# Kernel tuning notes

Hardware: AMD Instinct MI355X
Metric: run time of the kernel (lower is better)

The kernel has to match this reference:

```python
import jax, jax.numpy as jnp
import numpy as np

EPS = 1e-8
N_ITER = 3
S = 8      # n_slots
D = 64     # slot_size
HID = 128  # mlp hidden


def _ln(x, w, b):
    m = jnp.mean(x, axis=-1, keepdims=True)
    v = jnp.var(x, axis=-1, keepdims=True)
    return (x - m) * jax.lax.rsqrt(v + 1e-5) * w + b


def setup_inputs() -> dict:
    key = jax.random.key(0)
    ks = jax.random.split(key, 20)
    B, N, Din = 128, 4096, 64
    g = lambda k, sh, s: (jax.random.normal(k, sh, jnp.float32) * s)
    return {
        "inputs": jax.random.normal(ks[0], (B, N, Din), jnp.float32),
        "eps_noise": jax.random.normal(ks[1], (B, S, D), jnp.float32),
        "slot_mu": g(ks[2], (1, 1, D), 0.1),
        "slot_logvar": g(ks[3], (1, 1, D), 0.1),
        "k_w": g(ks[4], (D, Din), 1.0 / np.sqrt(Din)),
        "v_w": g(ks[5], (D, Din), 1.0 / np.sqrt(Din)),
        "q_w": g(ks[6], (D, D), 1.0 / np.sqrt(D)),
        "ni_w": jnp.ones((Din,), jnp.float32), "ni_b": jnp.zeros((Din,), jnp.float32),
        "ns_w": jnp.ones((D,), jnp.float32),  "ns_b": jnp.zeros((D,), jnp.float32),
        "nr_w": jnp.ones((D,), jnp.float32),  "nr_b": jnp.zeros((D,), jnp.float32),
        "gru_wih": g(ks[7], (3 * D, D), 1.0 / np.sqrt(D)),
        "gru_whh": g(ks[8], (3 * D, D), 1.0 / np.sqrt(D)),
        "gru_bih": jnp.zeros((3 * D,), jnp.float32),
        "gru_bhh": jnp.zeros((3 * D,), jnp.float32),
        "mlp_w1": g(ks[9], (HID, D), 1.0 / np.sqrt(D)),
        "mlp_w2": g(ks[10], (D, HID), 1.0 / np.sqrt(HID)),
        "mlp_b2": jnp.zeros((D,), jnp.float32),
    }


def _gru(x, h, wih, whh, bih, bhh):
    gi = x @ wih.T + bih  # [BS, 3D]
    gh = h @ whh.T + bhh
    i_r, i_z, i_n = jnp.split(gi, 3, axis=-1)
    h_r, h_z, h_n = jnp.split(gh, 3, axis=-1)
    r = jax.nn.sigmoid(i_r + h_r)
    z = jax.nn.sigmoid(i_z + h_z)
    n = jnp.tanh(i_n + r * h_n)
    return (1.0 - z) * n + z * h


def _step(slots, k, v, q_w, ns_w, ns_b, nr_w, nr_b,
          gru_wih, gru_whh, gru_bih, gru_bhh, mlp_w1, mlp_w2, mlp_b2):
    B = slots.shape[0]
    q = _ln(slots, ns_w, ns_b) @ q_w.T                     # [B,S,D]
    logits = jnp.einsum('bnd,bsd->bns', k, q)              # [B,N,S]
    w = jax.nn.softmax(logits, axis=-1) + EPS              # softmax over slots
    w = w / jnp.sum(w, axis=-2, keepdims=True)             # renorm over tokens
    atten_maps = jnp.einsum('bns,bnd->bsd', w, v)          # [B,S,D]
    h = _gru(atten_maps.reshape(B * S, D), slots.reshape(B * S, D),
             gru_wih, gru_whh, gru_bih, gru_bhh)
    h = h + (jax.nn.relu(_ln(h, nr_w, nr_b) @ mlp_w1.T) @ mlp_w2.T + mlp_b2)
    return h.reshape(B, S, D), w


def reference(inputs, eps_noise, slot_mu, slot_logvar, k_w, v_w, q_w,
              ni_w, ni_b, ns_w, ns_b, nr_w, nr_b,
              gru_wih, gru_whh, gru_bih, gru_bhh, mlp_w1, mlp_w2, mlp_b2):
    std = jnp.exp(0.5 * slot_logvar)
    slots = slot_mu + std * eps_noise                      # [B,S,D]
    x = _ln(inputs, ni_w, ni_b)
    k = (x @ k_w.T) / np.sqrt(D).astype(np.float32)        # [B,N,D]
    v = x @ v_w.T
    args = (q_w, ns_w, ns_b, nr_w, nr_b, gru_wih, gru_whh,
            gru_bih, gru_bhh, mlp_w1, mlp_w2, mlp_b2)
    for _ in range(N_ITER):
        slots, w = _step(slots, k, v, *args)
    slots, w = _step(jax.lax.stop_gradient(slots), k, v, *args)
    return slots, w
```

## Files before the change

kernel.cpp:

```cpp
#include <hip/hip_runtime.h>
#include <hip/hip_bf16.h>

#define BB 128
#define NN 4096
#define DD 64
#define SS 8
#define HH 128

typedef __attribute__((ext_vector_type(8))) short short8;
typedef __attribute__((ext_vector_type(4))) short short4v;
typedef __attribute__((ext_vector_type(4))) float f32x4;

__device__ __forceinline__ float warp_red_sum(float v) {
    #pragma unroll
    for (int off = 32; off; off >>= 1) v += __shfl_xor(v, off);
    return v;
}

__device__ __forceinline__ float bcastlane(float v, int l) {
    return __int_as_float(__builtin_amdgcn_readlane(__float_as_int(v), l));
}

__device__ __forceinline__ unsigned short bfu(float f) {
    __hip_bfloat16 h = __float2bfloat16(f);
    return *(unsigned short*)&h;
}

__device__ __forceinline__ unsigned pk2(float a, float b) {
    return (unsigned)bfu(a) | ((unsigned)bfu(b) << 16);
}

__device__ __forceinline__ short4v ds_tr16(unsigned off) {
    short4v r;
    asm volatile("ds_read_b64_tr_b16 %0, %1" : "=v"(r) : "v"(off));
    return r;
}

__global__ __launch_bounds__(256) void prep_kernel(
    const float* __restrict__ v_w, const float* __restrict__ q_w,
    const float* __restrict__ wih, const float* __restrict__ whh,
    const float* __restrict__ w1, const float* __restrict__ w2,
    float* __restrict__ vwT, float* __restrict__ qwT,
    float* __restrict__ wihT, float* __restrict__ whhT,
    float* __restrict__ w1T, float* __restrict__ w2T)
{
    int i0 = blockIdx.x * blockDim.x + threadIdx.x;
    int nthr = gridDim.x * blockDim.x;
    for (int t = i0; t < 4096; t += nthr) {
        int i = t >> 6, o = t & 63;
        vwT[t] = v_w[o * 64 + i];
        qwT[t] = q_w[o * 64 + i];
    }
    for (int t = i0; t < 12288; t += nthr) {
        int r = t / 192, c = t % 192;
        wihT[t] = wih[c * 64 + r];
        whhT[t] = whh[c * 64 + r];
    }
    for (int t = i0; t < 8192; t += nthr) {
        int r = t >> 7, c = t & 127;
        w1T[t] = w1[c * 64 + r];
    }
    for (int t = i0; t < 8192; t += nthr) {
        int r = t >> 6, c = t & 63;
        w2T[t] = w2[c * 128 + r];
    }
}

__global__ __launch_bounds__(256) void init_q_kernel(
    const float* __restrict__ eps, const float* __restrict__ mu,
    const float* __restrict__ lv, const float* __restrict__ qwT,
    const float* __restrict__ k_w,
    const float* __restrict__ nsw, const float* __restrict__ nsb,
    float* __restrict__ slots, unsigned short* __restrict__ qb,
    float* __restrict__ zbuf)
{
    const int tid = threadIdx.x, lane = tid & 63;
    const int row = blockIdx.x * 4 + (tid >> 6);
    const int idx = row * 64 + lane;
    float s0 = mu[lane] + __expf(0.5f * lv[lane]) * eps[idx];
    slots[idx] = s0;
    float m = warp_red_sum(s0) * (1.0f / 64.0f);
    float dx = s0 - m;
    float var = warp_red_sum(dx * dx) * (1.0f / 64.0f);
    float xln = dx * rsqrtf(var + 1e-5f) * nsw[lane] + nsb[lane];
    float q = 0.f;
    #pragma unroll 8
    for (int i = 0; i < 64; ++i) q = fmaf(bcastlane(xln, i), qwT[i * 64 + lane], q);
    float qp = 0.f;
    #pragma unroll 8
    for (int o = 0; o < 64; ++o) qp = fmaf(bcastlane(q, o), k_w[o * 64 + lane], qp);
    qb[idx] = bfu(qp * 0.125f);
    int g = blockIdx.x * 256 + tid;
    for (int j = g; j < 66560; j += 65536) zbuf[j] = 0.f;
}

__global__ __launch_bounds__(256) void phase_a_ln(
    const float* __restrict__ inp, const float* __restrict__ niw, const float* __restrict__ nib,
    unsigned short* __restrict__ xb)
{
    const int tid = threadIdx.x, lane = tid & 63, widx = tid >> 6;
    const int t8 = lane >> 3, d8 = lane & 7;
    const float4 wn0 = *(const float4*)&niw[d8 * 8];
    const float4 wn1 = *(const float4*)&niw[d8 * 8 + 4];
    const float4 bn0 = *(const float4*)&nib[d8 * 8];
    const float4 bn1 = *(const float4*)&nib[d8 * 8 + 4];
    const int tok0 = blockIdx.x * 128;
    #pragma unroll
    for (int it = 0; it < 4; ++it) {
        const int m = widx * 32 + it * 8 + t8;
        const float* rowp = inp + (size_t)(tok0 + m) * 64 + d8 * 8;
        float4 a = *(const float4*)rowp;
        float4 c = *(const float4*)(rowp + 4);
        float s1 = (a.x + a.y + a.z + a.w) + (c.x + c.y + c.z + c.w);
        float s2 = fmaf(a.x, a.x, fmaf(a.y, a.y, fmaf(a.z, a.z, a.w * a.w)));
        s2 = fmaf(c.x, c.x, fmaf(c.y, c.y, fmaf(c.z, c.z, fmaf(c.w, c.w, s2))));
        #pragma unroll
        for (int o = 1; o < 8; o <<= 1) { s1 += __shfl_xor(s1, o); s2 += __shfl_xor(s2, o); }
        float mean = s1 * (1.0f / 64.0f);
        float var = s2 * (1.0f / 64.0f) - mean * mean;
        float rstd = rsqrtf(var + 1e-5f);
        float y[8];
        y[0] = (a.x - mean) * rstd * wn0.x + bn0.x;
        y[1] = (a.y - mean) * rstd * wn0.y + bn0.y;
        y[2] = (a.z - mean) * rstd * wn0.z + bn0.z;
        y[3] = (a.w - mean) * rstd * wn0.w + bn0.w;
        y[4] = (c.x - mean) * rstd * wn1.x + bn1.x;
        y[5] = (c.y - mean) * rstd * wn1.y + bn1.y;
        y[6] = (c.z - mean) * rstd * wn1.z + bn1.z;
        y[7] = (c.w - mean) * rstd * wn1.w + bn1.w;
        uint4 o4;
        o4.x = pk2(y[0], y[1]); o4.y = pk2(y[2], y[3]);
        o4.z = pk2(y[4], y[5]); o4.w = pk2(y[6], y[7]);
        *(uint4*)&xb[(size_t)(tok0 + m) * 64 + d8 * 8] = o4;
    }
}

__global__ __launch_bounds__(256) void attn_mfma(
    const __hip_bfloat16* __restrict__ xb,
    const unsigned short* __restrict__ qb,
    float* __restrict__ numer, float* __restrict__ denom, float* __restrict__ wout)
{
    __shared__ unsigned short smem[11904];
    unsigned short* Qs = smem;
    const int tid = threadIdx.x, lane = tid & 63, widx = tid >> 6;
    unsigned short* wls = smem + 1152 + widx * 640;
    unsigned short* Xw  = smem + 3712 + widx * 2048;
    const int b = blockIdx.y;
    const int quad = lane >> 4, l16 = lane & 15;
    const int twave0 = blockIdx.x * 512 + widx * 128;

    short8 bkA[2][2], bkB[2][2];
    #pragma unroll
    for (int t4h = 0; t4h < 2; ++t4h) {
        const size_t xrow = ((size_t)b * NN + twave0 + t4h * 16 + l16) * 64;
        bkA[t4h][0] = *(const short8*)&xb[xrow + quad * 8];
        bkA[t4h][1] = *(const short8*)&xb[xrow + 32 + quad * 8];
    }

    for (int t = tid; t < 1024; t += 256) {
        int s = t >> 6, dd = t & 63;
        Qs[s * 72 + dd] = (s < 8) ? qb[b * 512 + t] : (unsigned short)0;
    }
    for (int t = lane; t < 320; t += 64) wls[320 + t] = 0;
    __syncthreads();

    short8 aq0 = *(const short8*)&Qs[l16 * 72 + quad * 8];
    short8 aq1 = *(const short8*)&Qs[l16 * 72 + 32 + quad * 8];

    f32x4 accv[4];
    #pragma unroll
    for (int nt = 0; nt < 4; ++nt) accv[nt] = (f32x4){0.f, 0.f, 0.f, 0.f};
    float dacc[4] = {0.f, 0.f, 0.f, 0.f};

    unsigned short* xw0 = Xw + (quad >> 1) * 512 + l16 * 16 + (quad & 1) * 8;
    const unsigned xtr = (unsigned)(size_t)Xw
                       + (unsigned)((quad * 8 + (l16 >> 2)) * 32 + (l16 & 3) * 8);

    auto PROC = [&](short8 (&cur)[2][2], short8 (&nxt)[2][2], int hg, bool pf) {
        const int t0g = twave0 + hg * 32;
        if (pf) {
            #pragma unroll
            for (int t4h = 0; t4h < 2; ++t4h) {
                const size_t xrow = ((size_t)b * NN + t0g + 32 + t4h * 16 + l16) * 64;
                nxt[t4h][0] = *(const short8*)&xb[xrow + quad * 8];
                nxt[t4h][1] = *(const short8*)&xb[xrow + 32 + quad * 8];
            }
        }
        #pragma unroll
        for (int t4h = 0; t4h < 2; ++t4h) {
            const int tok = t0g + t4h * 16 + l16;
            short8 bk0 = cur[t4h][0];
            short8 bk1 = cur[t4h][1];
            *(short8*)(xw0 + t4h * 256) = bk0;
            *(short8*)(xw0 + t4h * 256 + 1024) = bk1;
            f32x4 lg = (f32x4){0.f, 0.f, 0.f, 0.f};
            lg = __builtin_amdgcn_mfma_f32_16x16x32_bf16(aq0, bk0, lg, 0, 0, 0);
            lg = __builtin_amdgcn_mfma_f32_16x16x32_bf16(aq1, bk1, lg, 0, 0, 0);
            float e[4];
            #pragma unroll
            for (int r = 0; r < 4; ++r) e[r] = __expf(lg[r]);
            float s4 = (e[0] + e[1]) + (e[2] + e[3]);
            float stot = s4 + __shfl_xor(s4, 16);
            float rs = __builtin_amdgcn_rcpf(stot);
            float wv[4];
            #pragma unroll
            for (int r = 0; r < 4; ++r) { wv[r] = fmaf(e[r], rs, 1e-8f); dacc[r] += wv[r]; }
            if (quad < 2) {
                #pragma unroll
                for (int r = 0; r < 4; ++r)
                    wls[(quad * 4 + r) * 40 + t4h * 16 + l16] = bfu(wv[r]);
                if (wout)
                    *(float4*)&wout[((size_t)b * NN + tok) * 8 + quad * 4] =
                        make_float4(wv[0], wv[1], wv[2], wv[3]);
            }
        }
        asm volatile("" ::: "memory");
        short8 aw = *(const short8*)&wls[l16 * 40 + quad * 8];
        short4v rlo[4], rhi[4];
        #pragma unroll
        for (int nt = 0; nt < 4; ++nt) {
            rlo[nt] = ds_tr16(xtr + nt * 1024);
            rhi[nt] = ds_tr16(xtr + nt * 1024 + 128);
        }
        asm volatile("s_waitcnt lgkmcnt(0)");
        __builtin_amdgcn_sched_barrier(0);
        #pragma unroll
        for (int nt = 0; nt < 4; ++nt) {
            short8 bv = __builtin_shufflevector(rlo[nt], rhi[nt], 0, 1, 2, 3, 4, 5, 6, 7);
            accv[nt] = __builtin_amdgcn_mfma_f32_16x16x32_bf16(aw, bv, accv[nt], 0, 0, 0);
        }
    };

    PROC(bkA, bkB, 0, true);
    PROC(bkB, bkA, 1, true);
    PROC(bkA, bkB, 2, true);
    PROC(bkB, bkA, 3, false);

    #pragma unroll
    for (int r = 0; r < 4; ++r) {
        dacc[r] += __shfl_xor(dacc[r], 1);
        dacc[r] += __shfl_xor(dacc[r], 2);
        dacc[r] += __shfl_xor(dacc[r], 4);
        dacc[r] += __shfl_xor(dacc[r], 8);
    }
    __syncthreads();
    float* red = (float*)smem;
    float* dred = red + 2048;
    if (quad < 2) {
        #pragma unroll
        for (int nt = 0; nt < 4; ++nt)
            #pragma unroll
            for (int r = 0; r < 4; ++r)
                red[widx * 512 + (quad * 4 + r) * 64 + nt * 16 + l16] = accv[nt][r];
        if (l16 == 0) {
            #pragma unroll
            for (int r = 0; r < 4; ++r) dred[widx * 8 + quad * 4 + r] = dacc[r];
        }
    }
    __syncthreads();
    for (int e = tid; e < 512; e += 256)
        atomicAdd(numer + (size_t)b * 512 + e, red[e] + red[512 + e] + red[1024 + e] + red[1536 + e]);
    if (tid < 8)
        atomicAdd(denom + b * 8 + tid, dred[tid] + dred[8 + tid] + dred[16 + tid] + dred[24 + tid]);
}

__global__ __launch_bounds__(256) void gru_q_kernel(
    const float* __restrict__ numerX, const float* __restrict__ denom,
    const float* __restrict__ slotsIn,
    const float* __restrict__ vwT, const float* __restrict__ wihT, const float* __restrict__ whhT,
    const float* __restrict__ w1T, const float* __restrict__ w2T,
    const float* __restrict__ bih, const float* __restrict__ bhh,
    const float* __restrict__ nrw, const float* __restrict__ nrb,
    const float* __restrict__ b2,
    const float* __restrict__ qwT, const float* __restrict__ k_w,
    const float* __restrict__ nsw, const float* __restrict__ nsb,
    float* __restrict__ slotsOut, unsigned short* __restrict__ qb,
    float* __restrict__ zbuf)
{
    const int tid = threadIdx.x, lane = tid & 63;
    const int row = blockIdx.x * 4 + (tid >> 6);
    float nx = numerX[row * 64 + lane];
    float xp = 0.f;
    #pragma unroll 8
    for (int i = 0; i < 64; ++i) xp = fmaf(bcastlane(nx, i), vwT[i * 64 + lane], xp);
    float x = xp / denom[row];
    float h = slotsIn[row * 64 + lane];
    float air = 0, aiz = 0, ain = 0, ahr = 0, ahz = 0, ahn = 0;
    #pragma unroll 8
    for (int i = 0; i < 64; ++i) {
        float xi = bcastlane(x, i), hi = bcastlane(h, i);
        const float* wi = wihT + i * 192;
        const float* wh = whhT + i * 192;
        air = fmaf(xi, wi[lane], air);
        aiz = fmaf(xi, wi[64 + lane], aiz);
        ain = fmaf(xi, wi[128 + lane], ain);
        ahr = fmaf(hi, wh[lane], ahr);
        ahz = fmaf(hi, wh[64 + lane], ahz);
        ahn = fmaf(hi, wh[128 + lane], ahn);
    }
    air += bih[lane]; aiz += bih[64 + lane]; ain += bih[128 + lane];
    ahr += bhh[lane]; ahz += bhh[64 + lane]; ahn += bhh[128 + lane];
    float r = 1.f / (1.f + __expf(-(air + ahr)));
    float z = 1.f / (1.f + __expf(-(aiz + ahz)));
    float n = tanhf(ain + r * ahn);
    float hn = (1.f - z) * n + z * h;
    float m = warp_red_sum(hn) * (1.0f / 64.0f);
    float dx = hn - m;
    float var = warp_red_sum(dx * dx) * (1.0f / 64.0f);
    float u = dx * rsqrtf(var + 1e-5f) * nrw[lane] + nrb[lane];
    float o0 = 0.f, o1 = 0.f;
    #pragma unroll 8
    for (int i = 0; i < 64; ++i) {
        float ui = bcastlane(u, i);
        const float* w1r = w1T + i * 128;
        o0 = fmaf(ui, w1r[lane], o0);
        o1 = fmaf(ui, w1r[64 + lane], o1);
    }
    o0 = fmaxf(o0, 0.f); o1 = fmaxf(o1, 0.f);
    float y = 0.f;
    #pragma unroll 8
    for (int j = 0; j < 64; ++j) y = fmaf(bcastlane(o0, j), w2T[j * 64 + lane], y);
    #pragma unroll 8
    for (int j = 0; j < 64; ++j) y = fmaf(bcastlane(o1, j), w2T[(64 + j) * 64 + lane], y);
    y += b2[lane];
    float out = hn + y;
    slotsOut[row * 64 + lane] = out;
    float m2 = warp_red_sum(out) * (1.0f / 64.0f);
    float dx2 = out - m2;
    float var2 = warp_red_sum(dx2 * dx2) * (1.0f / 64.0f);
    float u2 = dx2 * rsqrtf(var2 + 1e-5f) * nsw[lane] + nsb[lane];
    float q = 0.f;
    #pragma unroll 8
    for (int i = 0; i < 64; ++i) q = fmaf(bcastlane(u2, i), qwT[i * 64 + lane], q);
    float qp = 0.f;
    #pragma unroll 8
    for (int o = 0; o < 64; ++o) qp = fmaf(bcastlane(q, o), k_w[o * 64 + lane], qp);
    qb[row * 64 + lane] = bfu(qp * 0.125f);
    int g = blockIdx.x * 256 + tid;
    for (int j = g; j < 66560; j += 65536) zbuf[j] = 0.f;
}

__global__ __launch_bounds__(256) void renorm_kernel(float* __restrict__ wout,
                                                     const float* __restrict__ denom)
{
    const size_t i4 = (size_t)blockIdx.x * blockDim.x + threadIdx.x;
    const size_t b = i4 >> 13;
    const int half = (int)(i4 & 1);
    float4 v = reinterpret_cast<float4*>(wout)[i4];
    const float4 dv = reinterpret_cast<const float4*>(denom)[b * 2 + half];
    v.x /= dv.x; v.y /= dv.y; v.z /= dv.z; v.w /= dv.w;
    reinterpret_cast<float4*>(wout)[i4] = v;
}

extern "C" void kernel_launch(void* const* d_in, const int* in_sizes, int n_in,
                              void* d_out, int out_size, void* d_ws, size_t ws_size,
                              hipStream_t stream)
{
    const float* inputs  = (const float*)d_in[0];
    const float* eps_n   = (const float*)d_in[1];
    const float* mu      = (const float*)d_in[2];
    const float* lv      = (const float*)d_in[3];
    const float* k_w     = (const float*)d_in[4];
    const float* v_w     = (const float*)d_in[5];
    const float* q_w     = (const float*)d_in[6];
    const float* ni_w    = (const float*)d_in[7];
    const float* ni_b    = (const float*)d_in[8];
    const float* ns_w    = (const float*)d_in[9];
    const float* ns_b    = (const float*)d_in[10];
    const float* nr_w    = (const float*)d_in[11];
    const float* nr_b    = (const float*)d_in[12];
    const float* gru_wih = (const float*)d_in[13];
    const float* gru_whh = (const float*)d_in[14];
    const float* gru_bih = (const float*)d_in[15];
    const float* gru_bhh = (const float*)d_in[16];
    const float* mlp_w1  = (const float*)d_in[17];
    const float* mlp_w2  = (const float*)d_in[18];
    const float* mlp_b2  = (const float*)d_in[19];

    char* wsb = (char*)d_ws;
    unsigned short* xb  = (unsigned short*)wsb;
    float* f      = (float*)(wsb + 134217728);
    float* slotsA = f;
    float* slotsB = f + 65536;
    unsigned short* qb = (unsigned short*)(f + 131072);
    float* numer0 = f + 163840;
    float* denom0 = f + 229376;
    float* numer1 = f + 230400;
    float* denom1 = f + 295936;
    float* vwT    = f + 296960;
    float* qwT    = f + 301056;
    float* wihT   = f + 305152;
    float* whhT   = f + 317440;
    float* w1T    = f + 329728;
    float* w2T    = f + 337920;

    float* out_slots = (float*)d_out;
    float* out_w     = out_slots + 65536;

    prep_kernel<<<64, 256, 0, stream>>>(v_w, q_w, gru_wih, gru_whh, mlp_w1, mlp_w2,
                                        vwT, qwT, wihT, whhT, w1T, w2T);
    init_q_kernel<<<256, 256, 0, stream>>>(eps_n, mu, lv, qwT, k_w, ns_w, ns_b,
                                           slotsA, qb, numer0);
    phase_a_ln<<<4096, 256, 0, stream>>>(inputs, ni_w, ni_b, xb);

    float* cur = slotsA;
    float* numers[2] = {numer0, numer1};
    float* denoms[2] = {denom0, denom1};
    for (int step = 0; step < 4; ++step) {
        int pb = step & 1;
        attn_mfma<<<dim3(8, 128), 256, 0, stream>>>((const __hip_bfloat16*)xb, qb,
                                                    numers[pb], denoms[pb],
                                                    step == 3 ? out_w : nullptr);
        float* nxt = (step == 3) ? out_slots : ((step & 1) ? slotsA : slotsB);
        gru_q_kernel<<<256, 256, 0, stream>>>(numers[pb], denoms[pb], cur,
                                              vwT, wihT, whhT, w1T, w2T,
                                              gru_bih, gru_bhh, nr_w, nr_b, mlp_b2,
                                              qwT, k_w, ns_w, ns_b,
                                              nxt, qb, numers[1 - pb]);
        cur = nxt;
    }
    renorm_kernel<<<4096, 256, 0, stream>>>(out_w, denom1);
}
```

Before: 390.3 us.

## Fuse prep kernels and replace atomic reductions with per-block partials

The three setup kernels (weight transposes, slot init with first query, input layernorm) are merged into one 4096-block launch, with block ranges assigned to each task. The attention kernel now writes per-block partial numerators and denominators instead of using atomicAdd. The GRU kernel sums the 8 partials itself, which removes the buffer zeroing and double buffering. This cuts launch count and atomic contention, but each GRU thread does more reads, and fused_pre blocks do uneven work.

```diff
diff --git a/kernel.cpp b/kernel.cpp
--- a/kernel.cpp
+++ b/kernel.cpp
@@ -36,75 +36,17 @@
     return r;
 }
 
-__global__ __launch_bounds__(256) void prep_kernel(
-    const float* __restrict__ v_w, const float* __restrict__ q_w,
-    const float* __restrict__ wih, const float* __restrict__ whh,
-    const float* __restrict__ w1, const float* __restrict__ w2,
-    float* __restrict__ vwT, float* __restrict__ qwT,
-    float* __restrict__ wihT, float* __restrict__ whhT,
-    float* __restrict__ w1T, float* __restrict__ w2T)
-{
-    int i0 = blockIdx.x * blockDim.x + threadIdx.x;
-    int nthr = gridDim.x * blockDim.x;
-    for (int t = i0; t < 4096; t += nthr) {
-        int i = t >> 6, o = t & 63;
-        vwT[t] = v_w[o * 64 + i];
-        qwT[t] = q_w[o * 64 + i];
-    }
-    for (int t = i0; t < 12288; t += nthr) {
-        int r = t / 192, c = t % 192;
-        wihT[t] = wih[c * 64 + r];
-        whhT[t] = whh[c * 64 + r];
-    }
-    for (int t = i0; t < 8192; t += nthr) {
-        int r = t >> 7, c = t & 127;
-        w1T[t] = w1[c * 64 + r];
-    }
-    for (int t = i0; t < 8192; t += nthr) {
-        int r = t >> 6, c = t & 63;
-        w2T[t] = w2[c * 128 + r];
-    }
-}
-
-__global__ __launch_bounds__(256) void init_q_kernel(
-    const float* __restrict__ eps, const float* __restrict__ mu,
-    const float* __restrict__ lv, const float* __restrict__ qwT,
-    const float* __restrict__ k_w,
-    const float* __restrict__ nsw, const float* __restrict__ nsb,
-    float* __restrict__ slots, unsigned short* __restrict__ qb,
-    float* __restrict__ zbuf)
-{
-    const int tid = threadIdx.x, lane = tid & 63;
-    const int row = blockIdx.x * 4 + (tid >> 6);
-    const int idx = row * 64 + lane;
-    float s0 = mu[lane] + __expf(0.5f * lv[lane]) * eps[idx];
-    slots[idx] = s0;
-    float m = warp_red_sum(s0) * (1.0f / 64.0f);
-    float dx = s0 - m;
-    float var = warp_red_sum(dx * dx) * (1.0f / 64.0f);
-    float xln = dx * rsqrtf(var + 1e-5f) * nsw[lane] + nsb[lane];
-    float q = 0.f;
-    #pragma unroll 8
-    for (int i = 0; i < 64; ++i) q = fmaf(bcastlane(xln, i), qwT[i * 64 + lane], q);
-    float qp = 0.f;
-    #pragma unroll 8
-    for (int o = 0; o < 64; ++o) qp = fmaf(bcastlane(q, o), k_w[o * 64 + lane], qp);
-    qb[idx] = bfu(qp * 0.125f);
-    int g = blockIdx.x * 256 + tid;
-    for (int j = g; j < 66560; j += 65536) zbuf[j] = 0.f;
-}
-
-__global__ __launch_bounds__(256) void phase_a_ln(
-    const float* __restrict__ inp, const float* __restrict__ niw, const float* __restrict__ nib,
-    unsigned short* __restrict__ xb)
-{
-    const int tid = threadIdx.x, lane = tid & 63, widx = tid >> 6;
+__device__ __forceinline__ void ln_block(
+    const float* __restrict__ inp, const float* __restrict__ niw,
+    const float* __restrict__ nib, unsigned short* __restrict__ xb,
+    int tok0, int tid)
+{
+    const int lane = tid & 63, widx = tid >> 6;
     const int t8 = lane >> 3, d8 = lane & 7;
     const float4 wn0 = *(const float4*)&niw[d8 * 8];
     const float4 wn1 = *(const float4*)&niw[d8 * 8 + 4];
     const float4 bn0 = *(const float4*)&nib[d8 * 8];
     const float4 bn1 = *(const float4*)&nib[d8 * 8 + 4];
-    const int tok0 = blockIdx.x * 128;
     #pragma unroll
     for (int it = 0; it < 4; ++it) {
         const int m = widx * 32 + it * 8 + t8;
@@ -135,10 +77,136 @@
     }
 }
 
+__device__ __forceinline__ void gru_core(
+    float nx, float dt, int row, int lane,
+    const float* __restrict__ vwT, const float* __restrict__ wihT,
+    const float* __restrict__ whhT, const float* __restrict__ w1T,
+    const float* __restrict__ w2T, const float* __restrict__ bih,
+    const float* __restrict__ bhh, const float* __restrict__ nrw,
+    const float* __restrict__ nrb, const float* __restrict__ b2,
+    const float* __restrict__ qwT, const float* __restrict__ k_w,
+    const float* __restrict__ nsw, const float* __restrict__ nsb,
+    const float* __restrict__ slotsIn, float* __restrict__ slotsOut,
+    unsigned short* __restrict__ qb)
+{
+    float xp = 0.f;
+    #pragma unroll 8
+    for (int i = 0; i < 64; ++i) xp = fmaf(bcastlane(nx, i), vwT[i * 64 + lane], xp);
+    float x = xp / dt;
+    float h = slotsIn[row * 64 + lane];
+    float air = 0, aiz = 0, ain = 0, ahr = 0, ahz = 0, ahn = 0;
+    #pragma unroll 8
+    for (int i = 0; i < 64; ++i) {
+        float xi = bcastlane(x, i), hi = bcastlane(h, i);
+        const float* wi = wihT + i * 192;
+        const float* wh = whhT + i * 192;
+        air = fmaf(xi, wi[lane], air);
+        aiz = fmaf(xi, wi[64 + lane], aiz);
+        ain = fmaf(xi, wi[128 + lane], ain);
+        ahr = fmaf(hi, wh[lane], ahr);
+        ahz = fmaf(hi, wh[64 + lane], ahz);
+        ahn = fmaf(hi, wh[128 + lane], ahn);
+    }
+    air += bih[lane]; aiz += bih[64 + lane]; ain += bih[128 + lane];
+    ahr += bhh[lane]; ahz += bhh[64 + lane]; ahn += bhh[128 + lane];
+    float r = 1.f / (1.f + __expf(-(air + ahr)));
+    float z = 1.f / (1.f + __expf(-(aiz + ahz)));
+    float n = tanhf(ain + r * ahn);
+    float hn = (1.f - z) * n + z * h;
+    float m = warp_red_sum(hn) * (1.0f / 64.0f);
+    float dx = hn - m;
+    float var = warp_red_sum(dx * dx) * (1.0f / 64.0f);
+    float u = dx * rsqrtf(var + 1e-5f) * nrw[lane] + nrb[lane];
+    float o0 = 0.f, o1 = 0.f;
+    #pragma unroll 8
+    for (int i = 0; i < 64; ++i) {
+        float ui = bcastlane(u, i);
+        const float* w1r = w1T + i * 128;
+        o0 = fmaf(ui, w1r[lane], o0);
+        o1 = fmaf(ui, w1r[64 + lane], o1);
+    }
+    o0 = fmaxf(o0, 0.f); o1 = fmaxf(o1, 0.f);
+    float y = 0.f;
+    #pragma unroll 8
+    for (int j = 0; j < 64; ++j) y = fmaf(bcastlane(o0, j), w2T[j * 64 + lane], y);
+    #pragma unroll 8
+    for (int j = 0; j < 64; ++j) y = fmaf(bcastlane(o1, j), w2T[(64 + j) * 64 + lane], y);
+    y += b2[lane];
+    float out = hn + y;
+    slotsOut[row * 64 + lane] = out;
+    float m2 = warp_red_sum(out) * (1.0f / 64.0f);
+    float dx2 = out - m2;
+    float var2 = warp_red_sum(dx2 * dx2) * (1.0f / 64.0f);
+    float u2 = dx2 * rsqrtf(var2 + 1e-5f) * nsw[lane] + nsb[lane];
+    float q = 0.f;
+    #pragma unroll 8
+    for (int i = 0; i < 64; ++i) q = fmaf(bcastlane(u2, i), qwT[i * 64 + lane], q);
+    float qp = 0.f;
+    #pragma unroll 8
+    for (int o = 0; o < 64; ++o) qp = fmaf(bcastlane(q, o), k_w[o * 64 + lane], qp);
+    qb[row * 64 + lane] = bfu(qp * 0.125f);
+}
+
+__global__ __launch_bounds__(256) void fused_pre(
+    const float* __restrict__ inp, const float* __restrict__ niw, const float* __restrict__ nib,
+    const float* __restrict__ eps, const float* __restrict__ mu, const float* __restrict__ lv,
+    const float* __restrict__ q_w, const float* __restrict__ k_w,
+    const float* __restrict__ nsw, const float* __restrict__ nsb,
+    const float* __restrict__ v_w, const float* __restrict__ wih, const float* __restrict__ whh,
+    const float* __restrict__ w1, const float* __restrict__ w2,
+    unsigned short* __restrict__ xb, unsigned short* __restrict__ qb,
+    float* __restrict__ slots,
+    float* __restrict__ vwT, float* __restrict__ qwT,
+    float* __restrict__ wihT, float* __restrict__ whhT,
+    float* __restrict__ w1T, float* __restrict__ w2T)
+{
+    const int bid = blockIdx.x, tid = threadIdx.x;
+    const int lane = tid & 63, widx = tid >> 6;
+    if (bid < 64) {
+        int i0 = bid * 256 + tid, nthr = 16384;
+        for (int t = i0; t < 4096; t += nthr) {
+            int i = t >> 6, o = t & 63;
+            vwT[t] = v_w[o * 64 + i];
+            qwT[t] = q_w[o * 64 + i];
+        }
+        for (int t = i0; t < 12288; t += nthr) {
+            int r = t / 192, c = t % 192;
+            wihT[t] = wih[c * 64 + r];
+            whhT[t] = whh[c * 64 + r];
+        }
+        for (int t = i0; t < 8192; t += nthr) {
+            int r = t >> 7, c = t & 127;
+            w1T[t] = w1[c * 64 + r];
+        }
+        for (int t = i0; t < 8192; t += nthr) {
+            int r = t >> 6, c = t & 63;
+            w2T[t] = w2[c * 128 + r];
+        }
+    }
+    ln_block(inp, niw, nib, xb, bid * 128, tid);
+    if (bid >= 64 && bid < 320) {
+        const int row = (bid - 64) * 4 + widx;
+        const int idx = row * 64 + lane;
+        float s0 = mu[lane] + __expf(0.5f * lv[lane]) * eps[idx];
+        slots[idx] = s0;
+        float m = warp_red_sum(s0) * (1.0f / 64.0f);
+        float dx = s0 - m;
+        float var = warp_red_sum(dx * dx) * (1.0f / 64.0f);
+        float xln = dx * rsqrtf(var + 1e-5f) * nsw[lane] + nsb[lane];
+        float q = 0.f;
+        #pragma unroll 8
+        for (int i = 0; i < 64; ++i) q = fmaf(bcastlane(xln, i), q_w[lane * 64 + i], q);
+        float qp = 0.f;
+        #pragma unroll 8
+        for (int o = 0; o < 64; ++o) qp = fmaf(bcastlane(q, o), k_w[o * 64 + lane], qp);
+        qb[idx] = bfu(qp * 0.125f);
+    }
+}
+
 __global__ __launch_bounds__(256) void attn_mfma(
     const __hip_bfloat16* __restrict__ xb,
     const unsigned short* __restrict__ qb,
-    float* __restrict__ numer, float* __restrict__ denom, float* __restrict__ wout)
+    float* __restrict__ numerP, float* __restrict__ denomP, float* __restrict__ wout)
 {
     __shared__ unsigned short smem[11904];
     unsigned short* Qs = smem;
@@ -258,14 +326,16 @@
         }
     }
     __syncthreads();
+    float* np = numerP + ((size_t)b * 8 + blockIdx.x) * 512;
     for (int e = tid; e < 512; e += 256)
-        atomicAdd(numer + (size_t)b * 512 + e, red[e] + red[512 + e] + red[1024 + e] + red[1536 + e]);
+        np[e] = red[e] + red[512 + e] + red[1024 + e] + red[1536 + e];
     if (tid < 8)
-        atomicAdd(denom + b * 8 + tid, dred[tid] + dred[8 + tid] + dred[16 + tid] + dred[24 + tid]);
+        denomP[((size_t)b * 8 + blockIdx.x) * 8 + tid] =
+            dred[tid] + dred[8 + tid] + dred[16 + tid] + dred[24 + tid];
 }
 
 __global__ __launch_bounds__(256) void gru_q_kernel(
-    const float* __restrict__ numerX, const float* __restrict__ denom,
+    const float* __restrict__ numerP, const float* __restrict__ denomP,
     const float* __restrict__ slotsIn,
     const float* __restrict__ vwT, const float* __restrict__ wihT, const float* __restrict__ whhT,
     const float* __restrict__ w1T, const float* __restrict__ w2T,
@@ -275,69 +345,20 @@
     const float* __restrict__ qwT, const float* __restrict__ k_w,
     const float* __restrict__ nsw, const float* __restrict__ nsb,
     float* __restrict__ slotsOut, unsigned short* __restrict__ qb,
-    float* __restrict__ zbuf)
+    float* __restrict__ denomF)
 {
     const int tid = threadIdx.x, lane = tid & 63;
     const int row = blockIdx.x * 4 + (tid >> 6);
-    float nx = numerX[row * 64 + lane];
-    float xp = 0.f;
-    #pragma unroll 8
-    for (int i = 0; i < 64; ++i) xp = fmaf(bcastlane(nx, i), vwT[i * 64 + lane], xp);
-    float x = xp / denom[row];
-    float h = slotsIn[row * 64 + lane];
-    float air = 0, aiz = 0, ain = 0, ahr = 0, ahz = 0, ahn = 0;
-    #pragma unroll 8
-    for (int i = 0; i < 64; ++i) {
-        float xi = bcastlane(x, i), hi = bcastlane(h, i);
-        const float* wi = wihT + i * 192;
-        const float* wh = whhT + i * 192;
-        air = fmaf(xi, wi[lane], air);
-        aiz = fmaf(xi, wi[64 + lane], aiz);
-        ain = fmaf(xi, wi[128 + lane], ain);
-        ahr = fmaf(hi, wh[lane], ahr);
-        ahz = fmaf(hi, wh[64 + lane], ahz);
-        ahn = fmaf(hi, wh[128 + lane], ahn);
-    }
-    air += bih[lane]; aiz += bih[64 + lane]; ain += bih[128 + lane];
-    ahr += bhh[lane]; ahz += bhh[64 + lane]; ahn += bhh[128 + lane];
-    float r = 1.f / (1.f + __expf(-(air + ahr)));
-    float z = 1.f / (1.f + __expf(-(aiz + ahz)));
-    float n = tanhf(ain + r * ahn);
-    float hn = (1.f - z) * n + z * h;
-    float m = warp_red_sum(hn) * (1.0f / 64.0f);
-    float dx = hn - m;
-    float var = warp_red_sum(dx * dx) * (1.0f / 64.0f);
-    float u = dx * rsqrtf(var + 1e-5f) * nrw[lane] + nrb[lane];
-    float o0 = 0.f, o1 = 0.f;
-    #pragma unroll 8
-    for (int i = 0; i < 64; ++i) {
-        float ui = bcastlane(u, i);
-        const float* w1r = w1T + i * 128;
-        o0 = fmaf(ui, w1r[lane], o0);
-        o1 = fmaf(ui, w1r[64 + lane], o1);
-    }
-    o0 = fmaxf(o0, 0.f); o1 = fmaxf(o1, 0.f);
-    float y = 0.f;
-    #pragma unroll 8
-    for (int j = 0; j < 64; ++j) y = fmaf(bcastlane(o0, j), w2T[j * 64 + lane], y);
-    #pragma unroll 8
-    for (int j = 0; j < 64; ++j) y = fmaf(bcastlane(o1, j), w2T[(64 + j) * 64 + lane], y);
-    y += b2[lane];
-    float out = hn + y;
-    slotsOut[row * 64 + lane] = out;
-    float m2 = warp_red_sum(out) * (1.0f / 64.0f);
-    float dx2 = out - m2;
-    float var2 = warp_red_sum(dx2 * dx2) * (1.0f / 64.0f);
-    float u2 = dx2 * rsqrtf(var2 + 1e-5f) * nsw[lane] + nsb[lane];
-    float q = 0.f;
-    #pragma unroll 8
-    for (int i = 0; i < 64; ++i) q = fmaf(bcastlane(u2, i), qwT[i * 64 + lane], q);
-    float qp = 0.f;
-    #pragma unroll 8
-    for (int o = 0; o < 64; ++o) qp = fmaf(bcastlane(q, o), k_w[o * 64 + lane], qp);
-    qb[row * 64 + lane] = bfu(qp * 0.125f);
-    int g = blockIdx.x * 256 + tid;
-    for (int j = g; j < 66560; j += 65536) zbuf[j] = 0.f;
+    const int bb = row >> 3, ss = row & 7;
+    float nx = 0.f, dt = 0.f;
+    #pragma unroll
+    for (int xx = 0; xx < 8; ++xx) {
+        nx += numerP[((size_t)bb * 8 + xx) * 512 + ss * 64 + lane];
+        dt += denomP[((size_t)bb * 8 + xx) * 8 + ss];
+    }
+    if (lane == 0) denomF[row] = dt;
+    gru_core(nx, dt, row, lane, vwT, wihT, whhT, w1T, w2T, bih, bhh, nrw, nrb, b2,
+             qwT, k_w, nsw, nsb, slotsIn, slotsOut, qb);
 }
 
 __global__ __launch_bounds__(256) void renorm_kernel(float* __restrict__ wout,
@@ -379,14 +400,14 @@
 
     char* wsb = (char*)d_ws;
     unsigned short* xb  = (unsigned short*)wsb;
+    float* P      = (float*)(wsb + 67108864);
+    float* numerP = P;
+    float* denomP = P + 524288;
+    float* denomF = P + 532480;
     float* f      = (float*)(wsb + 134217728);
     float* slotsA = f;
     float* slotsB = f + 65536;
     unsigned short* qb = (unsigned short*)(f + 131072);
-    float* numer0 = f + 163840;
-    float* denom0 = f + 229376;
-    float* numer1 = f + 230400;
-    float* denom1 = f + 295936;
     float* vwT    = f + 296960;
     float* qwT    = f + 301056;
     float* wihT   = f + 305152;
@@ -397,27 +418,24 @@
     float* out_slots = (float*)d_out;
     float* out_w     = out_slots + 65536;
 
-    prep_kernel<<<64, 256, 0, stream>>>(v_w, q_w, gru_wih, gru_whh, mlp_w1, mlp_w2,
+    fused_pre<<<4096, 256, 0, stream>>>(inputs, ni_w, ni_b, eps_n, mu, lv,
+                                        q_w, k_w, ns_w, ns_b,
+                                        v_w, gru_wih, gru_whh, mlp_w1, mlp_w2,
+                                        xb, qb, slotsA,
                                         vwT, qwT, wihT, whhT, w1T, w2T);
-    init_q_kernel<<<256, 256, 0, stream>>>(eps_n, mu, lv, qwT, k_w, ns_w, ns_b,
-                                           slotsA, qb, numer0);
-    phase_a_ln<<<4096, 256, 0, stream>>>(inputs, ni_w, ni_b, xb);
 
     float* cur = slotsA;
-    float* numers[2] = {numer0, numer1};
-    float* denoms[2] = {denom0, denom1};
     for (int step = 0; step < 4; ++step) {
-        int pb = step & 1;
         attn_mfma<<<dim3(8, 128), 256, 0, stream>>>((const __hip_bfloat16*)xb, qb,
-                                                    numers[pb], denoms[pb],
+                                                    numerP, denomP,
                                                     step == 3 ? out_w : nullptr);
         float* nxt = (step == 3) ? out_slots : ((step & 1) ? slotsA : slotsB);
-        gru_q_kernel<<<256, 256, 0, stream>>>(numers[pb], denoms[pb], cur,
+        gru_q_kernel<<<256, 256, 0, stream>>>(numerP, denomP, cur,
                                               vwT, wihT, whhT, w1T, w2T,
                                               gru_bih, gru_bhh, nr_w, nr_b, mlp_b2,
                                               qwT, k_w, ns_w, ns_b,
-                                              nxt, qb, numers[1 - pb]);
+                                              nxt, qb, denomF);
         cur = nxt;
     }
-    renorm_kernel<<<4096, 256, 0, stream>>>(out_w, denom1);
-}
+    renorm_kernel<<<4096, 256, 0, stream>>>(out_w, denomF);
+}
```

New measurement: 378.8 us. 3.0% less time.
